# Performance work log

Hardware: AMD Instinct MI355X
Metric: run time of the kernel (lower is better)

The kernel has to match this reference:

```python
import jax, jax.numpy as jnp
import numpy as np

B, S, D, P = 8, 2048, 1024, 32
H = 8
HD = D // H  # head_dim = 128


def setup_inputs() -> dict:
    key = jax.random.key(0)
    ks = jax.random.split(key, 14)
    x = jax.random.normal(ks[0], (B, S, D), dtype=jnp.float32)
    # 8 trigram projections, each Linear(D, HD, bias=False): stacked (H, HD, D)
    W_proj = jax.random.normal(ks[1], (H, HD, D), dtype=jnp.float32) * 0.02
    # resonance frequencies, init randn * 0.01 as in source
    freqs = jax.random.normal(ks[2], (H, HD), dtype=jnp.float32) * 0.01
    # per-head polarity generators Linear(HD, P) + Tanh
    Wp = jax.random.normal(ks[3], (H, P, HD), dtype=jnp.float32) * (1.0 / np.sqrt(HD))
    bp = jnp.zeros((H, P), dtype=jnp.float32)
    # impedance modulator: Linear(1,16) -> GELU -> Linear(16,1) -> Softplus
    w1 = jax.random.normal(ks[4], (16,), dtype=jnp.float32)
    b1 = jnp.zeros((16,), dtype=jnp.float32)
    w2 = jax.random.normal(ks[5], (16,), dtype=jnp.float32) * 0.25
    b2 = jnp.zeros((), dtype=jnp.float32)
    # output projection Linear(D, D) and LayerNorm(D)
    Wo = jax.random.normal(ks[6], (D, D), dtype=jnp.float32) * 0.02
    bo = jnp.zeros((D,), dtype=jnp.float32)
    ln_g = jnp.ones((D,), dtype=jnp.float32)
    ln_b = jnp.zeros((D,), dtype=jnp.float32)
    return {"x": x, "W_proj": W_proj, "freqs": freqs, "Wp": Wp, "bp": bp,
            "w1": w1, "b1": b1, "w2": w2, "b2": b2,
            "Wo": Wo, "bo": bo, "ln_g": ln_g, "ln_b": ln_b}


def reference(x, W_proj, freqs, Wp, bp, w1, b1, w2, b2, Wo, bo, ln_g, ln_b):
    # heads[i] = (x @ W_i^T) * cos(pi * freqs[i])  -> (B, H, S, HD)
    heads = jnp.einsum('bsd,hed->bhse', x, W_proj)
    heads = heads * jnp.cos(freqs * jnp.pi)[None, :, None, :]

    # --- GuaXiangDuiChong: impedance matrix (B, H, H) ---
    hm = heads.mean(axis=2)                                   # (B, H, HD)
    pv = jnp.tanh(jnp.einsum('bhd,hpd->bhp', hm, Wp) + bp[None])
    nrm = jnp.maximum(jnp.linalg.norm(pv, axis=-1, keepdims=True), 1e-12)
    pm = pv / nrm                                             # F.normalize
    dp = jnp.einsum('bip,bjp->bij', pm, pm)                   # (B, H, H)
    h1 = jax.nn.gelu(dp[..., None] * w1 + b1, approximate=False)  # (B,H,H,16)
    imp = jax.nn.softplus(jnp.einsum('bijk,k->bij', h1, w2) + b2)
    eye = jnp.eye(H, dtype=jnp.float32)
    impedance = imp * (1.0 - eye)[None]                       # zero diagonal

    # --- cross-head transfer with fused causal scaling ---
    # Original builds (B,S,S,HD) then masked mean over keys; mathematically
    # this equals scaling transfer[b,s,:] by (s+1)/S.
    coef = jnp.where(eye[None].astype(bool), 0.0, 0.1 / (1.0 + impedance))
    scale = (jnp.arange(S, dtype=jnp.float32) + 1.0) / S      # causal mean factor
    transfer = jnp.einsum('bij,bjse->bise', coef, heads) * scale[None, None, :, None]
    out_heads = heads + transfer                              # (B, H, S, HD)

    merged = out_heads.transpose(0, 2, 1, 3).reshape(B, S, D)
    y = merged @ Wo.T + bo + x                                # dropout = 0
    mu = y.mean(axis=-1, keepdims=True)
    var = ((y - mu) ** 2).mean(axis=-1, keepdims=True)
    y = (y - mu) * jax.lax.rsqrt(var + 1e-5) * ln_g + ln_b
    return y
```

## Files before the change

kernel.cpp:

```cpp
#include <hip/hip_runtime.h>
#include <hip/hip_bf16.h>

#define B_  8
#define S_  2048
#define D_  1024
#define H_  8
#define HD_ 128
#define P_  32
#define BS_ (B_*S_)
#define PI_F 3.14159265358979323846f

typedef unsigned short u16;
typedef __attribute__((ext_vector_type(4))) float  f32x4;
typedef __attribute__((ext_vector_type(8))) __bf16 bf16x8;
typedef __attribute__((ext_vector_type(8))) unsigned short u16x8;

__device__ __forceinline__ u16 f2b(float f) {
  __hip_bfloat16 h = __float2bfloat16(f);
  return __builtin_bit_cast(u16, h);
}
__device__ __forceinline__ float b2f(u16 b) {
  return __bfloat162float(__builtin_bit_cast(__hip_bfloat16, b));
}

__device__ __forceinline__ void gload_lds16(const void* g, void* l) {
  auto gp = (const __attribute__((address_space(1))) unsigned int*)g;
  auto lp = (__attribute__((address_space(3))) unsigned int*)l;
  __builtin_amdgcn_global_load_lds(gp, lp, 16, 0, 0);
}

__global__ __launch_bounds__(256) void cvt_x_kernel(const float* __restrict__ x,
                                                    u16* __restrict__ xb,
                                                    float* __restrict__ xsum) {
  const int r0 = blockIdx.x * 32;
  const int b = r0 >> 11;
  const int c = threadIdx.x * 4;
  float s0 = 0.f, s1 = 0.f, s2 = 0.f, s3 = 0.f;
#pragma unroll 4
  for (int i = 0; i < 32; ++i) {
    const float4 v = *reinterpret_cast<const float4*>(x + (size_t)(r0 + i) * D_ + c);
    ushort4 o;
    o.x = f2b(v.x); o.y = f2b(v.y); o.z = f2b(v.z); o.w = f2b(v.w);
    *reinterpret_cast<ushort4*>(xb + (size_t)(r0 + i) * D_ + c) = o;
    s0 += v.x; s1 += v.y; s2 += v.z; s3 += v.w;
  }
  atomicAdd(&xsum[b * D_ + c + 0], s0);
  atomicAdd(&xsum[b * D_ + c + 1], s1);
  atomicAdd(&xsum[b * D_ + c + 2], s2);
  atomicAdd(&xsum[b * D_ + c + 3], s3);
}

__global__ __launch_bounds__(256) void cvt_w_kernel(const float* __restrict__ Wproj,
                                                    const float* __restrict__ freqs,
                                                    const float* __restrict__ Wo,
                                                    u16* __restrict__ Wt1,
                                                    u16* __restrict__ Wob) {
  int i = blockIdx.x * blockDim.x + threadIdx.x;
  const int total = D_ * D_;
  for (; i < total; i += gridDim.x * blockDim.x) {
    int n = i >> 10;
    float c = cosf(PI_F * freqs[n]);
    Wt1[i] = f2b(Wproj[i] * c);
    Wob[i] = f2b(Wo[i]);
  }
}

__global__ __launch_bounds__(512, 2) void gemm256(const u16* __restrict__ A,
                                                  const u16* __restrict__ Bm,
                                                  u16* __restrict__ C,
                                                  int M, int N, int K) {
  __shared__ __align__(16) u16 lds[32768];
  const int tid = threadIdx.x;
  const int l = tid & 63, wid = tid >> 6;
  const int wm = wid >> 2, wn = wid & 3;
  const int bm0 = blockIdx.x * 256, bn0 = blockIdx.y * 256;

  const int gr = tid >> 2;
  const int gc = (tid & 3) ^ ((tid >> 3) & 3);
  const u16* pA1 = A  + (size_t)(bm0 + gr)       * K + gc * 8;
  const u16* pA2 = A  + (size_t)(bm0 + gr + 128) * K + gc * 8;
  const u16* pB1 = Bm + (size_t)(bn0 + gr)       * K + gc * 8;
  const u16* pB2 = Bm + (size_t)(bn0 + gr + 128) * K + gc * 8;

  const int lr = l & 15;
  const int cs = (l >> 4) ^ ((lr >> 1) & 3);

  f32x4 acc[8][4] = {};

  auto stage = [&](int buf) {
    u16* da = lds + buf * 8192;
    u16* db = lds + 16384 + buf * 8192;
    gload_lds16(pA1, da + tid * 8);
    gload_lds16(pA2, da + (512 + tid) * 8);
    gload_lds16(pB1, db + tid * 8);
    gload_lds16(pB2, db + (512 + tid) * 8);
    pA1 += 32; pA2 += 32; pB1 += 32; pB2 += 32;
  };

  auto compute = [&](int buf) {
    const u16* Ab = lds + buf * 8192;
    const u16* Bb = lds + 16384 + buf * 8192;
    bf16x8 af[8], bfr[4];
#pragma unroll
    for (int m = 0; m < 8; ++m)
      af[m] = *reinterpret_cast<const bf16x8*>(Ab + (wm * 128 + m * 16 + lr) * 32 + cs * 8);
#pragma unroll
    for (int n = 0; n < 4; ++n)
      bfr[n] = *reinterpret_cast<const bf16x8*>(Bb + (wn * 64 + n * 16 + lr) * 32 + cs * 8);
#pragma unroll
    for (int m = 0; m < 8; ++m)
#pragma unroll
      for (int n = 0; n < 4; ++n)
        acc[m][n] = __builtin_amdgcn_mfma_f32_16x16x32_bf16(af[m], bfr[n], acc[m][n], 0, 0, 0);
  };

  stage(0);
  __syncthreads();
  int cur = 0;
  const int NT = K / 32;
  for (int t = 0; t < NT - 1; ++t) {
    stage(cur ^ 1);
    compute(cur);
    __syncthreads();
    cur ^= 1;
  }
  compute(cur);

  const int jr = (l >> 4) * 4;
#pragma unroll
  for (int h = 0; h < 2; ++h) {
    __syncthreads();
    if (wm == h) {
#pragma unroll
      for (int m = 0; m < 8; ++m)
#pragma unroll
        for (int n = 0; n < 4; ++n)
#pragma unroll
          for (int j = 0; j < 4; ++j)
            lds[(m * 16 + jr + j) * 256 + wn * 64 + n * 16 + lr] = f2b(acc[m][n][j]);
    }
    __syncthreads();
#pragma unroll
    for (int i = 0; i < 8; ++i) {
      int g = tid + i * 512;
      int r = g >> 5, cg = g & 31;
      *reinterpret_cast<u16x8*>(C + (size_t)(bm0 + h * 128 + r) * N + bn0 + cg * 8) =
          *reinterpret_cast<const u16x8*>(lds + g * 8);
    }
  }
}

__global__ __launch_bounds__(256) void hm_gemv(const float* __restrict__ xsum,
                                               const u16* __restrict__ Wt1,
                                               float* __restrict__ hm) {
  const int gw = blockIdx.x * 4 + (threadIdx.x >> 6);
  const int b = gw >> 10, d = gw & 1023;
  const int lane = threadIdx.x & 63;
  const u16* wr = Wt1 + (size_t)d * D_ + lane * 16;
  const float* xs = xsum + b * D_ + lane * 16;
  u16x8 w0 = *reinterpret_cast<const u16x8*>(wr);
  u16x8 w1 = *reinterpret_cast<const u16x8*>(wr + 8);
  float4 x0 = reinterpret_cast<const float4*>(xs)[0];
  float4 x1 = reinterpret_cast<const float4*>(xs)[1];
  float4 x2 = reinterpret_cast<const float4*>(xs)[2];
  float4 x3 = reinterpret_cast<const float4*>(xs)[3];
  float s = 0.f;
  const float* xf = (const float*)&x0;
#pragma unroll
  for (int k = 0; k < 8; ++k) s += xf[k] * b2f(w0[k]);
  const float* xg = (const float*)&x2;
#pragma unroll
  for (int k = 0; k < 8; ++k) s += xg[k] * b2f(w1[k]);
  (void)x1; (void)x3;
#pragma unroll
  for (int off = 32; off; off >>= 1) s += __shfl_xor(s, off);
  if (lane == 0) hm[gw] = s * (1.0f / S_);
}

__global__ __launch_bounds__(256) void coef2_kernel(const float* __restrict__ hm,
                                                    const float* __restrict__ Wp,
                                                    const float* __restrict__ bp,
                                                    const float* __restrict__ w1,
                                                    const float* __restrict__ b1,
                                                    const float* __restrict__ w2,
                                                    const float* __restrict__ b2,
                                                    float* __restrict__ coef) {
  __shared__ float hm_s[D_];
  __shared__ float pm_s[H_ * P_];
  const int b = blockIdx.x, t = threadIdx.x;
#pragma unroll
  for (int q = 0; q < 4; ++q) hm_s[t * 4 + q] = hm[b * D_ + t * 4 + q];
  __syncthreads();
  {
    const int h = t >> 5, p = t & 31;
    float a = bp[h * P_ + p];
    const float* wp = Wp + (size_t)(h * P_ + p) * HD_;
#pragma unroll 4
    for (int e = 0; e < HD_; ++e) a += hm_s[h * HD_ + e] * wp[e];
    pm_s[t] = tanhf(a);
  }
  __syncthreads();
  if (t < 8) {
    float ss = 0.f;
    for (int p = 0; p < P_; ++p) { float v = pm_s[t * P_ + p]; ss += v * v; }
    float inv = 1.0f / fmaxf(sqrtf(ss), 1e-12f);
    for (int p = 0; p < P_; ++p) pm_s[t * P_ + p] *= inv;
  }
  __syncthreads();
  if (t < 64) {
    const int i = t >> 3, j = t & 7;
    float dp = 0.f;
    for (int p = 0; p < P_; ++p)
      dp += pm_s[i * P_ + p] * pm_s[j * P_ + p];
    float acc = b2[0];
#pragma unroll
    for (int k = 0; k < 16; ++k) {
      float z = dp * w1[k] + b1[k];
      float g = 0.5f * z * (1.0f + erff(z * 0.70710678118654752f));
      acc += g * w2[k];
    }
    float sp = (acc > 20.f) ? acc : log1pf(expf(acc));
    coef[b * 64 + t] = (i == j) ? 0.f : 0.1f / (1.0f + sp);
  }
}

__global__ __launch_bounds__(256) void mix_kernel(const u16* __restrict__ heads,
                                                  const float* __restrict__ coef,
                                                  u16* __restrict__ mixed) {
  __shared__ float row[D_];
  __shared__ float cf[64];
  const int r = blockIdx.x;
  const int b = r >> 11, s = r & 2047;
  const int t = threadIdx.x;
  if (t < 64) cf[t] = coef[b * 64 + t];
  const u16* hp = heads + (size_t)r * D_;
  ushort4 hv = reinterpret_cast<const ushort4*>(hp)[t];
#pragma unroll
  for (int q = 0; q < 4; ++q) row[t * 4 + q] = b2f(((u16*)&hv)[q]);
  __syncthreads();
  const float scale = (float)(s + 1) * (1.0f / S_);
  const int d0 = t * 4;
  const int h = d0 >> 7;
  float ch[8];
#pragma unroll
  for (int j = 0; j < 8; ++j) ch[j] = cf[h * 8 + j];
  ushort4 o;
#pragma unroll
  for (int q = 0; q < 4; ++q) {
    int d = d0 + q, e = d & 127;
    float tr = 0.f;
#pragma unroll
    for (int j = 0; j < 8; ++j) tr += ch[j] * row[j * 128 + e];
    ((u16*)&o)[q] = f2b(row[d] + scale * tr);
  }
  reinterpret_cast<ushort4*>(mixed + (size_t)r * D_)[t] = o;
}

__global__ __launch_bounds__(256) void ln_kernel(const u16* __restrict__ ypre,
                                                 const float* __restrict__ x,
                                                 const float* __restrict__ bo,
                                                 const float* __restrict__ g,
                                                 const float* __restrict__ be,
                                                 float* __restrict__ out) {
  const int r = blockIdx.x, t = threadIdx.x;
  const u16* yp = ypre + (size_t)r * D_;
  const float* xp = x + (size_t)r * D_;
  const int d0 = t * 4;
  float4 xv = reinterpret_cast<const float4*>(xp)[t];
  ushort4 yv = reinterpret_cast<const ushort4*>(yp)[t];
  float v[4];
  float s = 0.f, ss = 0.f;
#pragma unroll
  for (int q = 0; q < 4; ++q) {
    float y = b2f(((u16*)&yv)[q]) + bo[d0 + q] + ((const float*)&xv)[q];
    v[q] = y; s += y; ss += y * y;
  }
#pragma unroll
  for (int off = 32; off; off >>= 1) {
    s += __shfl_xor(s, off);
    ss += __shfl_xor(ss, off);
  }
  __shared__ float rs[4], rss[4];
  int w = t >> 6;
  if ((t & 63) == 0) { rs[w] = s; rss[w] = ss; }
  __syncthreads();
  s = rs[0] + rs[1] + rs[2] + rs[3];
  ss = rss[0] + rss[1] + rss[2] + rss[3];
  float mu = s * (1.0f / D_);
  float var = ss * (1.0f / D_) - mu * mu;
  float rstd = rsqrtf(var + 1e-5f);
  float4 ov;
#pragma unroll
  for (int q = 0; q < 4; ++q)
    ((float*)&ov)[q] = (v[q] - mu) * rstd * g[d0 + q] + be[d0 + q];
  reinterpret_cast<float4*>(out + (size_t)r * D_)[t] = ov;
}

extern "C" void kernel_launch(void* const* d_in, const int* in_sizes, int n_in,
                              void* d_out, int out_size, void* d_ws, size_t ws_size,
                              hipStream_t stream) {
  (void)in_sizes; (void)n_in; (void)out_size; (void)ws_size;
  const float* x     = (const float*)d_in[0];
  const float* Wproj = (const float*)d_in[1];
  const float* freqs = (const float*)d_in[2];
  const float* Wp    = (const float*)d_in[3];
  const float* bp    = (const float*)d_in[4];
  const float* w1    = (const float*)d_in[5];
  const float* b1    = (const float*)d_in[6];
  const float* w2    = (const float*)d_in[7];
  const float* b2    = (const float*)d_in[8];
  const float* Wo    = (const float*)d_in[9];
  const float* bo    = (const float*)d_in[10];
  const float* ln_g  = (const float*)d_in[11];
  const float* ln_b  = (const float*)d_in[12];
  float* out = (float*)d_out;

  char* ws = (char*)d_ws;
  u16*   xbf   = (u16*)ws;
  u16*   heads = (u16*)(ws + 33554432);
  u16*   Wt1   = (u16*)(ws + 67108864);
  u16*   Wob   = (u16*)(ws + 69206016);
  float* xsum  = (float*)(ws + 71303168);
  float* hm    = (float*)(ws + 71335936);
  float* coef  = (float*)(ws + 71368704);

  hipMemsetAsync(xsum, 0, B_ * D_ * sizeof(float), stream);

  cvt_x_kernel<<<512, 256, 0, stream>>>(x, xbf, xsum);
  cvt_w_kernel<<<1024, 256, 0, stream>>>(Wproj, freqs, Wo, Wt1, Wob);

  hm_gemv<<<2048, 256, 0, stream>>>(xsum, Wt1, hm);
  coef2_kernel<<<8, 256, 0, stream>>>(hm, Wp, bp, w1, b1, w2, b2, coef);

  dim3 g1(BS_ / 256, D_ / 256);
  gemm256<<<g1, 512, 0, stream>>>(xbf, Wt1, heads, BS_, D_, D_);

  mix_kernel<<<BS_, 256, 0, stream>>>(heads, coef, xbf );

  gemm256<<<g1, 512, 0, stream>>>(xbf, Wob, heads , BS_, D_, D_);

  ln_kernel<<<BS_, 256, 0, stream>>>(heads, x, bo, ln_g, ln_b, out);
}
```

Before: 270.3 us.

## Rewrite GEMM as 8-phase pipelined kernel with K=64 tiles; vectorize mix kernel

The 256x256 bf16 GEMM changes from a simple double-buffered K=32 loop to K=64 tiles in 128KB of dynamic LDS. The work is split into four quarter-tile MFMA phases, interleaved with staged global-to-LDS loads, explicit barriers, waitcnts and setprio, to overlap memory traffic with matrix math. The mix kernel now handles four rows per block, one wave per row, using register-resident head values instead of an LDS row buffer. The large LDS footprint may limit occupancy to one block per CU, and the hand-tuned waitcnt counts must stay correct.

After: 267.5 us. Within noise of the previous version (-1.0%).

```diff
diff --git a/kernel.cpp b/kernel.cpp
--- a/kernel.cpp
+++ b/kernel.cpp
@@ -11,6 +11,7 @@
 #define PI_F 3.14159265358979323846f
 
 typedef unsigned short u16;
+typedef unsigned int u32;
 typedef __attribute__((ext_vector_type(4))) float  f32x4;
 typedef __attribute__((ext_vector_type(8))) __bf16 bf16x8;
 typedef __attribute__((ext_vector_type(8))) unsigned short u16x8;
@@ -28,6 +29,15 @@
   auto lp = (__attribute__((address_space(3))) unsigned int*)l;
   __builtin_amdgcn_global_load_lds(gp, lp, 16, 0, 0);
 }
+
+#define FENCE() asm volatile("" ::: "memory")
+#define BAR() do { FENCE(); __builtin_amdgcn_sched_barrier(0); \
+                   __builtin_amdgcn_s_barrier(); \
+                   __builtin_amdgcn_sched_barrier(0); FENCE(); } while (0)
+#define LGKM0() do { asm volatile("s_waitcnt lgkmcnt(0)" ::: "memory"); \
+                     __builtin_amdgcn_sched_barrier(0); } while (0)
+#define VMC(N) do { asm volatile("s_waitcnt vmcnt(" #N ")" ::: "memory"); \
+                    __builtin_amdgcn_sched_barrier(0); } while (0)
 
 __global__ __launch_bounds__(256) void cvt_x_kernel(const float* __restrict__ x,
                                                     u16* __restrict__ xb,
@@ -65,66 +75,106 @@
   }
 }
 
-__global__ __launch_bounds__(512, 2) void gemm256(const u16* __restrict__ A,
-                                                  const u16* __restrict__ Bm,
-                                                  u16* __restrict__ C,
-                                                  int M, int N, int K) {
-  __shared__ __align__(16) u16 lds[32768];
+__global__ __launch_bounds__(512, 2) void gemm8p(const u16* __restrict__ A,
+                                                 const u16* __restrict__ Bm,
+                                                 u16* __restrict__ C,
+                                                 int M, int N, int K) {
+  extern __shared__ __align__(16) u16 smem[];
   const int tid = threadIdx.x;
-  const int l = tid & 63, wid = tid >> 6;
+  const int l = tid & 63;
+  const int wid = tid >> 6;
   const int wm = wid >> 2, wn = wid & 3;
+  const int lr = l & 15, lg = l >> 4;
   const int bm0 = blockIdx.x * 256, bn0 = blockIdx.y * 256;
 
-  const int gr = tid >> 2;
-  const int gc = (tid & 3) ^ ((tid >> 3) & 3);
-  const u16* pA1 = A  + (size_t)(bm0 + gr)       * K + gc * 8;
-  const u16* pA2 = A  + (size_t)(bm0 + gr + 128) * K + gc * 8;
-  const u16* pB1 = Bm + (size_t)(bn0 + gr)       * K + gc * 8;
-  const u16* pB2 = Bm + (size_t)(bn0 + gr + 128) * K + gc * 8;
-
-  const int lr = l & 15;
-  const int cs = (l >> 4) ^ ((lr >> 1) & 3);
+  const int srow = tid >> 3;
+  const int scol = ((tid & 7) ^ (srow & 7)) * 8;
 
   f32x4 acc[8][4] = {};
-
-  auto stage = [&](int buf) {
-    u16* da = lds + buf * 8192;
-    u16* db = lds + 16384 + buf * 8192;
-    gload_lds16(pA1, da + tid * 8);
-    gload_lds16(pA2, da + (512 + tid) * 8);
-    gload_lds16(pB1, db + tid * 8);
-    gload_lds16(pB2, db + (512 + tid) * 8);
-    pA1 += 32; pA2 += 32; pB1 += 32; pB2 += 32;
-  };
-
-  auto compute = [&](int buf) {
-    const u16* Ab = lds + buf * 8192;
-    const u16* Bb = lds + 16384 + buf * 8192;
-    bf16x8 af[8], bfr[4];
-#pragma unroll
-    for (int m = 0; m < 8; ++m)
-      af[m] = *reinterpret_cast<const bf16x8*>(Ab + (wm * 128 + m * 16 + lr) * 32 + cs * 8);
-#pragma unroll
-    for (int n = 0; n < 4; ++n)
-      bfr[n] = *reinterpret_cast<const bf16x8*>(Bb + (wn * 64 + n * 16 + lr) * 32 + cs * 8);
-#pragma unroll
-    for (int m = 0; m < 8; ++m)
-#pragma unroll
-      for (int n = 0; n < 4; ++n)
-        acc[m][n] = __builtin_amdgcn_mfma_f32_16x16x32_bf16(af[m], bfr[n], acc[m][n], 0, 0, 0);
-  };
-
-  stage(0);
-  __syncthreads();
-  int cur = 0;
-  const int NT = K / 32;
-  for (int t = 0; t < NT - 1; ++t) {
-    stage(cur ^ 1);
-    compute(cur);
-    __syncthreads();
-    cur ^= 1;
-  }
-  compute(cur);
+  bf16x8 af[4][2], b0[2][2], b1[2][2];
+
+  u16* const As = smem;
+  u16* const Bs = smem + 32768;
+
+  auto stageA = [&](int half, int kt, int buf) {
+    const u16* src = A + (size_t)(bm0 + half * 128 + srow) * K + kt * 64 + scol;
+    u16* dst = As + buf * 16384 + half * 8192 + tid * 8;
+    gload_lds16(src, dst);
+    gload_lds16(src + (size_t)64 * K, dst + 4096);
+  };
+  auto stageB = [&](int half, int kt, int buf) {
+    const u16* src = Bm + (size_t)(bn0 + half * 128 + srow) * K + kt * 64 + scol;
+    u16* dst = Bs + buf * 16384 + half * 8192 + tid * 8;
+    gload_lds16(src, dst);
+    gload_lds16(src + (size_t)64 * K, dst + 4096);
+  };
+  auto readA = [&](int buf, int mh) {
+#pragma unroll
+    for (int mi = 0; mi < 4; ++mi)
+#pragma unroll
+      for (int kk = 0; kk < 2; ++kk) {
+        int r = wm * 128 + mh * 64 + mi * 16 + lr;
+        int g = (kk * 4 + lg) ^ (lr & 7);
+        af[mi][kk] = *reinterpret_cast<const bf16x8*>(As + buf * 16384 + r * 64 + g * 8);
+      }
+  };
+  auto readB = [&](bf16x8 (&bb)[2][2], int buf, int nh) {
+#pragma unroll
+    for (int ni = 0; ni < 2; ++ni)
+#pragma unroll
+      for (int kk = 0; kk < 2; ++kk) {
+        int r = wn * 64 + (nh * 2 + ni) * 16 + lr;
+        int g = (kk * 4 + lg) ^ (lr & 7);
+        bb[ni][kk] = *reinterpret_cast<const bf16x8*>(Bs + buf * 16384 + r * 64 + g * 8);
+      }
+  };
+  auto mmaq = [&](int mh, int nh, bf16x8 (&bb)[2][2]) {
+    __builtin_amdgcn_s_setprio(1);
+#pragma unroll
+    for (int mi = 0; mi < 4; ++mi)
+#pragma unroll
+      for (int ni = 0; ni < 2; ++ni)
+#pragma unroll
+        for (int kk = 0; kk < 2; ++kk)
+          acc[mh * 4 + mi][nh * 2 + ni] = __builtin_amdgcn_mfma_f32_16x16x32_bf16(
+              af[mi][kk], bb[ni][kk], acc[mh * 4 + mi][nh * 2 + ni], 0, 0, 0);
+    __builtin_amdgcn_s_setprio(0);
+  };
+
+  const int NT = K >> 6;
+
+  stageA(0, 0, 0); stageB(0, 0, 0); stageA(1, 0, 0); stageB(1, 0, 0);
+  stageA(0, 1, 1); stageB(0, 1, 1); stageA(1, 1, 1);
+  VMC(6); BAR();
+
+  auto tile = [&](int u, int buf) {
+    readA(buf, 0); readB(b0, buf, 0);
+    if (u + 1 < NT) stageB(1, u + 1, buf ^ 1);
+    BAR(); LGKM0();
+    mmaq(0, 0, b0);
+    BAR();
+    readB(b1, buf, 1);
+    BAR(); LGKM0();
+    mmaq(0, 1, b1);
+    BAR();
+    readA(buf, 1);
+    if (u + 2 < NT) stageB(0, u + 2, buf);
+    BAR(); LGKM0();
+    mmaq(1, 0, b0);
+    BAR();
+    if (u + 2 < NT) { stageA(0, u + 2, buf); stageA(1, u + 2, buf); }
+    BAR(); LGKM0();
+    mmaq(1, 1, b1);
+    if (u + 1 < NT) {
+      if (u + 2 < NT) { VMC(6); } else { VMC(0); }
+    }
+    BAR();
+  };
+
+  for (int u = 0; u < NT; u += 2) {
+    tile(u, 0);
+    tile(u + 1, 1);
+  }
 
   const int jr = (l >> 4) * 4;
 #pragma unroll
@@ -137,7 +187,7 @@
         for (int n = 0; n < 4; ++n)
 #pragma unroll
           for (int j = 0; j < 4; ++j)
-            lds[(m * 16 + jr + j) * 256 + wn * 64 + n * 16 + lr] = f2b(acc[m][n][j]);
+            smem[(m * 16 + jr + j) * 256 + wn * 64 + n * 16 + lr] = f2b(acc[m][n][j]);
     }
     __syncthreads();
 #pragma unroll
@@ -145,7 +195,7 @@
       int g = tid + i * 512;
       int r = g >> 5, cg = g & 31;
       *reinterpret_cast<u16x8*>(C + (size_t)(bm0 + h * 128 + r) * N + bn0 + cg * 8) =
-          *reinterpret_cast<const u16x8*>(lds + g * 8);
+          *reinterpret_cast<const u16x8*>(smem + g * 8);
     }
   }
 }
@@ -227,33 +277,34 @@
 __global__ __launch_bounds__(256) void mix_kernel(const u16* __restrict__ heads,
                                                   const float* __restrict__ coef,
                                                   u16* __restrict__ mixed) {
-  __shared__ float row[D_];
-  __shared__ float cf[64];
-  const int r = blockIdx.x;
-  const int b = r >> 11, s = r & 2047;
-  const int t = threadIdx.x;
-  if (t < 64) cf[t] = coef[b * 64 + t];
-  const u16* hp = heads + (size_t)r * D_;
-  ushort4 hv = reinterpret_cast<const ushort4*>(hp)[t];
-#pragma unroll
-  for (int q = 0; q < 4; ++q) row[t * 4 + q] = b2f(((u16*)&hv)[q]);
-  __syncthreads();
+  __shared__ float cfs[64];
+  const int r = blockIdx.x * 4 + (threadIdx.x >> 6);
+  const int b = blockIdx.x >> 9;
+  const int s = r & 2047;
+  const int t = threadIdx.x & 63;
+  if (threadIdx.x < 64) cfs[threadIdx.x] = coef[b * 64 + threadIdx.x];
+  __syncthreads();
+  const u16* hp = heads + (size_t)r * D_ + 2 * t;
+  float hx[8], hy[8];
+#pragma unroll
+  for (int j = 0; j < 8; ++j) {
+    u32 v = *reinterpret_cast<const u32*>(hp + j * 128);
+    hx[j] = b2f((u16)(v & 0xffff));
+    hy[j] = b2f((u16)(v >> 16));
+  }
   const float scale = (float)(s + 1) * (1.0f / S_);
-  const int d0 = t * 4;
-  const int h = d0 >> 7;
-  float ch[8];
-#pragma unroll
-  for (int j = 0; j < 8; ++j) ch[j] = cf[h * 8 + j];
-  ushort4 o;
-#pragma unroll
-  for (int q = 0; q < 4; ++q) {
-    int d = d0 + q, e = d & 127;
-    float tr = 0.f;
-#pragma unroll
-    for (int j = 0; j < 8; ++j) tr += ch[j] * row[j * 128 + e];
-    ((u16*)&o)[q] = f2b(row[d] + scale * tr);
-  }
-  reinterpret_cast<ushort4*>(mixed + (size_t)r * D_)[t] = o;
+  u16* op = mixed + (size_t)r * D_ + 2 * t;
+#pragma unroll
+  for (int i = 0; i < 8; ++i) {
+    float tx = 0.f, ty = 0.f;
+#pragma unroll
+    for (int j = 0; j < 8; ++j) {
+      float c = cfs[i * 8 + j];
+      tx += c * hx[j]; ty += c * hy[j];
+    }
+    u32 o = (u32)f2b(hx[i] + scale * tx) | ((u32)f2b(hy[i] + scale * ty) << 16);
+    *reinterpret_cast<u32*>(op + i * 128) = o;
+  }
 }
 
 __global__ __launch_bounds__(256) void ln_kernel(const u16* __restrict__ ypre,
@@ -324,6 +375,9 @@
   float* hm    = (float*)(ws + 71335936);
   float* coef  = (float*)(ws + 71368704);
 
+  hipFuncSetAttribute((const void*)gemm8p,
+                      hipFuncAttributeMaxDynamicSharedMemorySize, 131072);
+
   hipMemsetAsync(xsum, 0, B_ * D_ * sizeof(float), stream);
 
   cvt_x_kernel<<<512, 256, 0, stream>>>(x, xbf, xsum);
@@ -333,11 +387,11 @@
   coef2_kernel<<<8, 256, 0, stream>>>(hm, Wp, bp, w1, b1, w2, b2, coef);
 
   dim3 g1(BS_ / 256, D_ / 256);
-  gemm256<<<g1, 512, 0, stream>>>(xbf, Wt1, heads, BS_, D_, D_);
-
-  mix_kernel<<<BS_, 256, 0, stream>>>(heads, coef, xbf );
-
-  gemm256<<<g1, 512, 0, stream>>>(xbf, Wob, heads , BS_, D_, D_);
+  gemm8p<<<g1, 512, 131072, stream>>>(xbf, Wt1, heads, BS_, D_, D_);
+
+  mix_kernel<<<BS_ / 4, 256, 0, stream>>>(heads, coef, xbf );
+
+  gemm8p<<<g1, 512, 131072, stream>>>(xbf, Wob, heads , BS_, D_, D_);
 
   ln_kernel<<<BS_, 256, 0, stream>>>(heads, x, bo, ln_g, ln_b, out);
 }
```
